# Kernel tuning notes

Hardware: AMD Instinct MI355X
Metric: run time of the kernel (lower is better)

Reference implementation:

```python
import jax, jax.numpy as jnp
import numpy as np

D_IN = 1024
D_OUT = 1024


def setup_inputs() -> dict:
    key = jax.random.key(0)
    kx, kq, kk, kv = jax.random.split(key, 4)
    x = jax.random.normal(kx, (4, 2048, D_IN), dtype=jnp.float32)
    s = 1.0 / np.sqrt(D_IN)
    Wq = jax.random.normal(kq, (D_IN, D_OUT), dtype=jnp.float32) * s
    Wk = jax.random.normal(kk, (D_IN, D_OUT), dtype=jnp.float32) * s
    Wv = jax.random.normal(kv, (D_IN, D_OUT), dtype=jnp.float32) * s
    return {"x": x, "Wq": Wq, "Wk": Wk, "Wv": Wv}


def reference(x, Wq, Wk, Wv):
    # x: [B, S, d_in]; W*: [d_in, d_out]
    B, S, _ = x.shape
    q = x @ Wq  # [B, S, d_out]
    k = x @ Wk
    v = x @ Wv
    scale = 1.0 / jnp.sqrt(jnp.asarray(k.shape[-1], x.dtype))
    scores = jnp.einsum("bqd,bkd->bqk", q, k) * scale  # [B, S, S]
    # causal mask: positions j > i masked to -inf (triu, diagonal=1)
    causal = jnp.tril(jnp.ones((S, S), dtype=bool))
    scores = jnp.where(causal[None, :, :], scores, -jnp.inf)
    attn = jax.nn.softmax(scores, axis=-1)  # dropout p=0.0 -> identity
    return jnp.einsum("bqk,bkd->bqd", attn, v)
```

## Files before the change

### kernel.cpp

```cpp
#include <hip/hip_runtime.h>
#include <hip/hip_bf16.h>

#define NB 4
#define SB 2048
#define DD 1024
#define BM 128
#define BN 128
#define BK 32

typedef __attribute__((ext_vector_type(8))) short bf16x8;
typedef __attribute__((ext_vector_type(4))) short bf16x4;
typedef __attribute__((ext_vector_type(4))) float f32x4;
typedef unsigned int u32;

__device__ __forceinline__ float bf2f(unsigned short u) {
    return __uint_as_float(((u32)u) << 16);
}
__device__ __forceinline__ short f2bf(float f) {
    u32 u = __float_as_uint(f);
    u32 r = (u + 0x7fffu + ((u >> 16) & 1u)) >> 16;
    return (short)r;
}

__device__ __forceinline__ void wait_vm6() {
    asm volatile("s_waitcnt vmcnt(6)" ::: "memory");
}
__device__ __forceinline__ void wait_vm0() {
    asm volatile("s_waitcnt vmcnt(0)" ::: "memory");
}
__device__ __forceinline__ void barrier_raw() {
    __builtin_amdgcn_s_barrier();
    asm volatile("" ::: "memory");
}

__device__ __forceinline__ void mfma_step(const short* As, const short* Bs,
                                          f32x4 (&acc)[4][4], int lane, int wave)
{
    const int wm = (wave >> 1) * 64, wn = (wave & 1) * 64;
    const int fr = lane & 15;
    const int quad = lane >> 4;
    bf16x8 af[4], bf[4];
#pragma unroll
    for (int t = 0; t < 4; t++) {
        af[t] = *(const bf16x8*)&As[(wm + t * 16 + fr) * BK + quad * 8];
        bf[t] = *(const bf16x8*)&Bs[(wn + t * 16 + fr) * BK + quad * 8];
    }
#pragma unroll
    for (int mt = 0; mt < 4; mt++)
#pragma unroll
        for (int nt = 0; nt < 4; nt++)
            acc[mt][nt] = __builtin_amdgcn_mfma_f32_16x16x32_bf16(
                af[mt], bf[nt], acc[mt][nt], 0, 0, 0);
}

__device__ __forceinline__ void mfma_step_pv(const short* As, const short* Bs,
                                             f32x4 (&acc)[2][4], int lane,
                                             int wave)
{
    const int wm = wave * 32;
    const int fr = lane & 15;
    const int quad = lane >> 4;
    bf16x8 af[2], bf[4];
#pragma unroll
    for (int t = 0; t < 2; t++)
        af[t] = *(const bf16x8*)&As[(wm + t * 16 + fr) * BK + quad * 8];
#pragma unroll
    for (int t = 0; t < 4; t++)
        bf[t] = *(const bf16x8*)&Bs[(t * 16 + fr) * BK + quad * 8];
#pragma unroll
    for (int mt = 0; mt < 2; mt++)
#pragma unroll
        for (int nt = 0; nt < 4; nt++)
            acc[mt][nt] = __builtin_amdgcn_mfma_f32_16x16x32_bf16(
                af[mt], bf[nt], acc[mt][nt], 0, 0, 0);
}

__device__ __forceinline__ void stage128x32(const short* __restrict__ g, int ld,
                                            short* lds, int tid) {
    const int wave = tid >> 6, lane = tid & 63;
    const int r = lane >> 2;
    const int c = (lane & 3) * 8;
#pragma unroll
    for (int i = 0; i < 2; i++) {
        const int chunk = wave * 2 + i;
        const short* gp = g + (size_t)(chunk * 16 + r) * ld + c;
        __builtin_amdgcn_global_load_lds(
            (const __attribute__((address_space(1))) u32*)gp,
            (__attribute__((address_space(3))) u32*)(lds + chunk * 512 + lane * 8),
            16, 0, 0);
    }
}

__device__ __forceinline__ void stage64x32(const short* __restrict__ g, int ld,
                                           short* lds, int tid) {
    const int wave = tid >> 6, lane = tid & 63;
    const int r = lane >> 2;
    const int c = (lane & 3) * 8;
    const short* gp = g + (size_t)(wave * 16 + r) * ld + c;
    __builtin_amdgcn_global_load_lds(
        (const __attribute__((address_space(1))) u32*)gp,
        (__attribute__((address_space(3))) u32*)(lds + wave * 512 + lane * 8),
        16, 0, 0);
}

__device__ __forceinline__ void stage_f32_128x32(const float* __restrict__ g,
                                                 int ld, short* lds, int tid) {
    const int r = tid >> 1;
    const int c = (tid & 1) * 16;
    const float* gp = &g[(size_t)r * ld + c];
    float4 v0 = *(const float4*)(gp + 0);
    float4 v1 = *(const float4*)(gp + 4);
    float4 v2 = *(const float4*)(gp + 8);
    float4 v3 = *(const float4*)(gp + 12);
    bf16x8 o0, o1;
    o0[0] = f2bf(v0.x); o0[1] = f2bf(v0.y); o0[2] = f2bf(v0.z); o0[3] = f2bf(v0.w);
    o0[4] = f2bf(v1.x); o0[5] = f2bf(v1.y); o0[6] = f2bf(v1.z); o0[7] = f2bf(v1.w);
    o1[0] = f2bf(v2.x); o1[1] = f2bf(v2.y); o1[2] = f2bf(v2.z); o1[3] = f2bf(v2.w);
    o1[4] = f2bf(v3.x); o1[5] = f2bf(v3.y); o1[6] = f2bf(v3.z); o1[7] = f2bf(v3.w);
    *(bf16x8*)&lds[r * BK + c] = o0;
    *(bf16x8*)&lds[r * BK + c + 8] = o1;
}

__device__ __forceinline__ void gemm_bt_body2(
    const short* __restrict__ A, int lda, const short* __restrict__ Bt, int ldb,
    int m0, int n0, int kend, short* As, short* Bs, f32x4 (&acc)[4][4], int tid)
{
    const int lane = tid & 63;
    const int wave = tid >> 6;
    const short* Ap = A + (size_t)m0 * lda;
    const short* Bp = Bt + (size_t)n0 * ldb;
    for (int k0 = 0; k0 < kend; k0 += 2 * BK) {
        stage128x32(Ap + k0, lda, As, tid);
        stage128x32(Ap + k0 + BK, lda, As + BM * BK, tid);
        stage128x32(Bp + k0, ldb, Bs, tid);
        stage128x32(Bp + k0 + BK, ldb, Bs + BN * BK, tid);
        __syncthreads();
        mfma_step(As, Bs, acc, lane, wave);
        mfma_step(As + BM * BK, Bs + BN * BK, acc, lane, wave);
        __syncthreads();
    }
}

__global__ __launch_bounds__(256) void prep_mm(
    const float* __restrict__ x, const float* __restrict__ Wq,
    const float* __restrict__ Wk, const float* __restrict__ Wv,
    short* __restrict__ xb, short* __restrict__ Wvt, float* __restrict__ Mp4)
{
    __shared__ short As[BM * BK], Bs[BN * BK];
    __shared__ short t[64][65];
    const int bx = blockIdx.x;
    const int tid = threadIdx.x;
    if (bx < 256) {
        const int ch = bx >> 6;
        const int t64 = bx & 63;
        const int m0 = (t64 >> 3) * BM;
        const int n0 = (t64 & 7) * BN;
        const int kbase = ch * 256;
        const int lane = tid & 63, wave = tid >> 6;
        f32x4 acc[4][4];
#pragma unroll
        for (int a = 0; a < 4; a++)
#pragma unroll
            for (int b = 0; b < 4; b++) acc[a][b] = (f32x4){0.f, 0.f, 0.f, 0.f};
        for (int k0 = 0; k0 < 256; k0 += BK) {
            stage_f32_128x32(Wk + (size_t)m0 * DD + kbase + k0, DD, As, tid);
            stage_f32_128x32(Wq + (size_t)n0 * DD + kbase + k0, DD, Bs, tid);
            __syncthreads();
            mfma_step(As, Bs, acc, lane, wave);
            __syncthreads();
        }
        const int wm = (wave >> 1) * 64, wn = (wave & 1) * 64;
        const int fr = lane & 15, quad = lane >> 4;
        float* Mc = Mp4 + (size_t)ch * DD * DD;
#pragma unroll
        for (int mt = 0; mt < 4; mt++)
#pragma unroll
            for (int nt = 0; nt < 4; nt++)
#pragma unroll
                for (int r = 0; r < 4; r++) {
                    const size_t m = m0 + wm + mt * 16 + quad * 4 + r;
                    const size_t n = n0 + wn + nt * 16 + fr;
                    Mc[m * DD + n] = acc[mt][nt][r];
                }
        return;
    }
    if (bx < 4352) {
        const size_t i = ((size_t)(bx - 256) * 256 + tid) * 8;
        float4 a = *(const float4*)&x[i];
        float4 b = *(const float4*)&x[i + 4];
        bf16x8 o;
        o[0] = f2bf(a.x); o[1] = f2bf(a.y); o[2] = f2bf(a.z); o[3] = f2bf(a.w);
        o[4] = f2bf(b.x); o[5] = f2bf(b.y); o[6] = f2bf(b.z); o[7] = f2bf(b.w);
        *(bf16x8*)&xb[i] = o;
        return;
    }
    const int rr = bx - 4352;
    const int k0 = (rr & 15) * 64;
    const int n0 = (rr >> 4) * 64;
    {
        const int r = tid >> 4;
        const int c = (tid & 15) * 4;
#pragma unroll
        for (int i = 0; i < 4; i++) {
            float4 v = *(const float4*)&Wv[(size_t)(k0 + i * 16 + r) * DD + n0 + c];
            t[i * 16 + r][c + 0] = f2bf(v.x);
            t[i * 16 + r][c + 1] = f2bf(v.y);
            t[i * 16 + r][c + 2] = f2bf(v.z);
            t[i * 16 + r][c + 3] = f2bf(v.w);
        }
    }
    __syncthreads();
    {
        const int r = tid >> 3;
        const int c = (tid & 7) * 8;
#pragma unroll
        for (int i = 0; i < 2; i++) {
            bf16x8 o;
#pragma unroll
            for (int j = 0; j < 8; j++) o[j] = t[c + j][i * 32 + r];
            *(bf16x8*)&Wvt[(size_t)(n0 + i * 32 + r) * DD + k0 + c] = o;
        }
    }
}

__global__ __launch_bounds__(256) void mm_reduce(const float* __restrict__ Mp4,
                                                 short* __restrict__ Mp)
{
    const size_t e = ((size_t)blockIdx.x * 256 + threadIdx.x) * 4;
    const size_t N = (size_t)DD * DD;
    float4 s = *(const float4*)&Mp4[e];
#pragma unroll
    for (int c = 1; c < 4; c++) {
        float4 p = *(const float4*)&Mp4[c * N + e];
        s.x += p.x; s.y += p.y; s.z += p.z; s.w += p.w;
    }
    bf16x4 o;
    o[0] = f2bf(s.x); o[1] = f2bf(s.y); o[2] = f2bf(s.z); o[3] = f2bf(s.w);
    *(bf16x4*)&Mp[e] = o;
}

__global__ __launch_bounds__(256) void tv_gemm(
    const short* __restrict__ xb, const short* __restrict__ Mp,
    const short* __restrict__ Wvt, short* __restrict__ T,
    short* __restrict__ Vt)
{
    __shared__ short As[2 * BM * BK], Bs[2 * BN * BK];
    const int lin = blockIdx.x + 8 * blockIdx.y;
    const int swz = (lin & 7) * 64 + (lin >> 3);
    const int n0 = (swz & 7) * BN;
    const int m0 = (swz >> 3) * BM;
    const int isv = blockIdx.z;
    const short* Bt = isv ? Wvt : Mp;
    f32x4 acc[4][4];
#pragma unroll
    for (int a = 0; a < 4; a++)
#pragma unroll
        for (int b = 0; b < 4; b++) acc[a][b] = (f32x4){0.f, 0.f, 0.f, 0.f};
    gemm_bt_body2(xb, DD, Bt, DD, m0, n0, DD, As, Bs, acc, threadIdx.x);
    const int lane = threadIdx.x & 63, wave = threadIdx.x >> 6;
    const int wm = (wave >> 1) * 64, wn = (wave & 1) * 64;
    const int fr = lane & 15, quad = lane >> 4;
    if (!isv) {
#pragma unroll
        for (int mt = 0; mt < 4; mt++)
#pragma unroll
            for (int nt = 0; nt < 4; nt++)
#pragma unroll
                for (int r = 0; r < 4; r++) {
                    const size_t m = m0 + wm + mt * 16 + quad * 4 + r;
                    const size_t n = n0 + wn + nt * 16 + fr;
                    T[m * DD + n] = f2bf(acc[mt][nt][r]);
                }
    } else {
        const int bb = m0 >> 11;
        const int s0 = (m0 & (SB - 1)) + wm + quad * 4;
        short* Vb = Vt + (size_t)bb * DD * SB;
#pragma unroll
        for (int mt = 0; mt < 4; mt++)
#pragma unroll
            for (int nt = 0; nt < 4; nt++) {
                const size_t n = n0 + wn + nt * 16 + fr;
                const size_t s = s0 + mt * 16;
                bf16x4 o;
#pragma unroll
                for (int r = 0; r < 4; r++) o[r] = f2bf(acc[mt][nt][r]);
                *(bf16x4*)&Vb[n * SB + s] = o;
            }
    }
}

__global__ __launch_bounds__(256) void scores_mfma(
    const short* __restrict__ T, const short* __restrict__ xb,
    short* __restrict__ Sc)
{
    const int bx = blockIdx.x;
    const int idx = (bx & 7) * 34 + (bx >> 3);
    int qt = (int)((__fsqrt_rn(4.f * idx + 1.f) - 1.f) * 0.5f);
    while ((qt + 1) * (qt + 2) <= idx) qt++;
    while (qt * (qt + 1) > idx) qt--;
    const int kt = idx - qt * (qt + 1);
    const int qm0 = qt * BM;
    const int kn0 = kt * 64;
    const int b = blockIdx.y;
    __shared__ short As[2 * BM * BK], Bs[2 * 64 * BK];
    const short* Tq = T + (size_t)b * SB * DD + (size_t)qm0 * DD;
    const short* Xk = xb + (size_t)b * SB * DD + (size_t)kn0 * DD;
    short* Sb = Sc + (size_t)b * SB * SB;
    const int tid = threadIdx.x;
    const int lane = tid & 63, wave = tid >> 6;
    f32x4 acc[2][4];
#pragma unroll
    for (int a = 0; a < 2; a++)
#pragma unroll
        for (int c = 0; c < 4; c++) acc[a][c] = (f32x4){0.f, 0.f, 0.f, 0.f};
    for (int k0 = 0; k0 < DD; k0 += 2 * BK) {
        stage128x32(Tq + k0, DD, As, tid);
        stage128x32(Tq + k0 + BK, DD, As + BM * BK, tid);
        stage64x32(Xk + k0, DD, Bs, tid);
        stage64x32(Xk + k0 + BK, DD, Bs + 64 * BK, tid);
        __syncthreads();
        mfma_step_pv(As, Bs, acc, lane, wave);
        mfma_step_pv(As + BM * BK, Bs + 64 * BK, acc, lane, wave);
        __syncthreads();
    }
    const int fr = lane & 15, quad = lane >> 4;
    const float scale = 0.03125f;
#pragma unroll
    for (int mt = 0; mt < 2; mt++)
#pragma unroll
        for (int nt = 0; nt < 4; nt++)
#pragma unroll
            for (int r = 0; r < 4; r++) {
                const size_t q = qm0 + wave * 32 + mt * 16 + quad * 4 + r;
                const size_t k = kn0 + nt * 16 + fr;
                Sb[q * SB + k] = f2bf(acc[mt][nt][r] * scale);
            }
}

__global__ __launch_bounds__(256) void softmax_kernel(short* __restrict__ Sc)
{
    const int row = blockIdx.x;
    const int i = row & (SB - 1);
    const int jlim = ((i >> 7) + 1) << 7;
    short* r = Sc + (size_t)row * SB;
    const int t = threadIdx.x;
    const int lane = t & 63, wave = t >> 6;
    __shared__ float red[8];

    const int j0 = t * 8;
    bf16x8 in = {0, 0, 0, 0, 0, 0, 0, 0};
    if (j0 <= i) in = *(const bf16x8*)&r[j0];
    float v[8];
    float mx = -1e30f;
#pragma unroll
    for (int e = 0; e < 8; e++) {
        const float s = (j0 + e <= i) ? bf2f((unsigned short)in[e]) : -1e30f;
        v[e] = s;
        mx = fmaxf(mx, s);
    }
#pragma unroll
    for (int o = 32; o > 0; o >>= 1) mx = fmaxf(mx, __shfl_down(mx, o));
    if (lane == 0) red[wave] = mx;
    __syncthreads();
    mx = fmaxf(fmaxf(red[0], red[1]), fmaxf(red[2], red[3]));

    float sum = 0.f;
#pragma unroll
    for (int e = 0; e < 8; e++) {
        const float x = (j0 + e <= i) ? __expf(v[e] - mx) : 0.f;
        v[e] = x;
        sum += x;
    }
#pragma unroll
    for (int o = 32; o > 0; o >>= 1) sum += __shfl_down(sum, o);
    if (lane == 0) red[4 + wave] = sum;
    __syncthreads();
    const float inv = 1.0f / (red[4] + red[5] + red[6] + red[7]);
    if (j0 < jlim) {
        bf16x8 o;
#pragma unroll
        for (int e = 0; e < 8; e++) o[e] = f2bf(v[e] * inv);
        *(bf16x8*)&r[j0] = o;
    }
}

__global__ __launch_bounds__(256) void pv_mfma(
    const short* __restrict__ P, const short* __restrict__ Vt,
    float* __restrict__ O)
{
    __shared__ short As[4 * BM * BK];
    __shared__ short Bs[4 * 64 * BK];
    const int n0 = blockIdx.x * 64;
    const int pair = blockIdx.y;
    const int b = blockIdx.z;
    const short* Pb = P + (size_t)b * SB * SB;
    const short* Vb = Vt + (size_t)b * DD * SB;
    float* Ob = O + (size_t)b * SB * DD;
    const int tid = threadIdx.x;
    const int lane = tid & 63, wave = tid >> 6;
    const int fr = lane & 15, quad = lane >> 4;
    for (int half = 0; half < 2; ++half) {
        const int qt = half ? (15 - pair) : pair;
        const int qm0 = qt * BM;
        const int nj = (qt + 1) * 2;
        const short* Pq = Pb + (size_t)qm0 * SB;
        const short* Vn = Vb + (size_t)n0 * SB;
        f32x4 acc[2][4];
#pragma unroll
        for (int a = 0; a < 2; a++)
#pragma unroll
            for (int c = 0; c < 4; c++) acc[a][c] = (f32x4){0.f, 0.f, 0.f, 0.f};
        stage128x32(Pq, SB, As, tid);
        stage128x32(Pq + BK, SB, As + BM * BK, tid);
        stage64x32(Vn, SB, Bs, tid);
        stage64x32(Vn + BK, SB, Bs + 64 * BK, tid);
        for (int j = 0; j < nj; ++j) {
            const int cur = j & 1;
            const short* as = As + cur * (2 * BM * BK);
            const short* bs = Bs + cur * (2 * 64 * BK);
            if (j + 1 < nj) {
                const int off = (j + 1) * 64;
                short* an = As + (cur ^ 1) * (2 * BM * BK);
                short* bn = Bs + (cur ^ 1) * (2 * 64 * BK);
                stage128x32(Pq + off, SB, an, tid);
                stage128x32(Pq + off + BK, SB, an + BM * BK, tid);
                stage64x32(Vn + off, SB, bn, tid);
                stage64x32(Vn + off + BK, SB, bn + 64 * BK, tid);
                wait_vm6();
            } else {
                wait_vm0();
            }
            barrier_raw();
            mfma_step_pv(as, bs, acc, lane, wave);
            mfma_step_pv(as + BM * BK, bs + 64 * BK, acc, lane, wave);
            barrier_raw();
        }
#pragma unroll
        for (int mt = 0; mt < 2; mt++)
#pragma unroll
            for (int nt = 0; nt < 4; nt++)
#pragma unroll
                for (int r = 0; r < 4; r++) {
                    const size_t q = qm0 + wave * 32 + mt * 16 + quad * 4 + r;
                    const size_t n = n0 + nt * 16 + fr;
                    Ob[q * DD + n] = acc[mt][nt][r];
                }
    }
}

extern "C" void kernel_launch(void* const* d_in, const int* in_sizes, int n_in,
                              void* d_out, int out_size, void* d_ws, size_t ws_size,
                              hipStream_t stream)
{
    const float* x  = (const float*)d_in[0];
    const float* Wq = (const float*)d_in[1];
    const float* Wk = (const float*)d_in[2];
    const float* Wv = (const float*)d_in[3];
    float* out = (float*)d_out;

    const size_t XE = (size_t)NB * SB * DD;
    const size_t WE = (size_t)DD * DD;
    short* xb  = (short*)d_ws;
    short* T   = xb + XE;
    short* Vt  = T + XE;
    short* Sc  = Vt + XE;
    float* Pp  = (float*)(Sc + (size_t)NB * SB * SB);
    short* Wvt = (short*)(Pp + (size_t)NB * 1024 * DD);
    short* Mp  = Wvt + WE;
    float* Mp4 = (float*)Sc;

    prep_mm<<<dim3(256 + 4096 + 256), 256, 0, stream>>>(
        x, Wq, Wk, Wv, xb, Wvt, Mp4);
    mm_reduce<<<dim3(1024), 256, 0, stream>>>(Mp4, Mp);
    tv_gemm<<<dim3(DD / BN, (NB * SB) / BM, 2), 256, 0, stream>>>(
        xb, Mp, Wvt, T, Vt);
    scores_mfma<<<dim3(272, NB), 256, 0, stream>>>(T, xb, Sc);
    softmax_kernel<<<dim3(NB * SB), 256, 0, stream>>>(Sc);
    pv_mfma<<<dim3(DD / 64, 8, NB), 256, 0, stream>>>(Sc, Vt, out);
}
```

Baseline: 231.0 us.

## Retile the projection GEMM to 256x128 with a three-stage async LDS pipeline

The projection GEMM kernel moves from 128x128 tiles with 256 threads to 256x128 tiles with 512 threads (8 waves). Each stage now holds a 64-wide K slice, and the stages rotate through three LDS buffers. Global-to-LDS loads for step j+2 are issued before computing step j, using counted vmcnt waits instead of a full sync. The MFMA section runs at raised wave priority. The aim is to hide global load latency and improve operand reuse, at the cost of about 147KB of LDS, which allows only one block per CU.

```diff
diff --git a/kernel.cpp b/kernel.cpp
--- a/kernel.cpp
+++ b/kernel.cpp
@@ -22,6 +22,9 @@
     return (short)r;
 }
 
+__device__ __forceinline__ void wait_vm12() {
+    asm volatile("s_waitcnt vmcnt(12)" ::: "memory");
+}
 __device__ __forceinline__ void wait_vm6() {
     asm volatile("s_waitcnt vmcnt(6)" ::: "memory");
 }
@@ -101,6 +104,35 @@
         (const __attribute__((address_space(1))) u32*)gp,
         (__attribute__((address_space(3))) u32*)(lds + wave * 512 + lane * 8),
         16, 0, 0);
+}
+
+__device__ __forceinline__ void stage_tile256(const short* __restrict__ gA,
+                                              int lda,
+                                              const short* __restrict__ gB,
+                                              int ldb, short* slot, int tid) {
+    const int w = tid >> 6, l = tid & 63;
+    const int lr = l >> 2;
+    const int lc = (l & 3) * 8;
+#pragma unroll
+    for (int i = 0; i < 4; i++) {
+        const int ks = i >> 1;
+        const int row = (i & 1) * 128 + w * 16 + lr;
+        const short* gp = gA + (size_t)row * lda + ks * 32 + lc;
+        __builtin_amdgcn_global_load_lds(
+            (const __attribute__((address_space(1))) u32*)gp,
+            (__attribute__((address_space(3))) u32*)(slot + i * 4096 + w * 512 + l * 8),
+            16, 0, 0);
+    }
+    short* bbase = slot + 16384;
+#pragma unroll
+    for (int i = 0; i < 2; i++) {
+        const int row = w * 16 + lr;
+        const short* gp = gB + (size_t)row * ldb + i * 32 + lc;
+        __builtin_amdgcn_global_load_lds(
+            (const __attribute__((address_space(1))) u32*)gp,
+            (__attribute__((address_space(3))) u32*)(bbase + i * 4096 + w * 512 + l * 8),
+            16, 0, 0);
+    }
 }
 
 __device__ __forceinline__ void stage_f32_128x32(const float* __restrict__ g,
@@ -121,26 +153,6 @@
     *(bf16x8*)&lds[r * BK + c + 8] = o1;
 }
 
-__device__ __forceinline__ void gemm_bt_body2(
-    const short* __restrict__ A, int lda, const short* __restrict__ Bt, int ldb,
-    int m0, int n0, int kend, short* As, short* Bs, f32x4 (&acc)[4][4], int tid)
-{
-    const int lane = tid & 63;
-    const int wave = tid >> 6;
-    const short* Ap = A + (size_t)m0 * lda;
-    const short* Bp = Bt + (size_t)n0 * ldb;
-    for (int k0 = 0; k0 < kend; k0 += 2 * BK) {
-        stage128x32(Ap + k0, lda, As, tid);
-        stage128x32(Ap + k0 + BK, lda, As + BM * BK, tid);
-        stage128x32(Bp + k0, ldb, Bs, tid);
-        stage128x32(Bp + k0 + BK, ldb, Bs + BN * BK, tid);
-        __syncthreads();
-        mfma_step(As, Bs, acc, lane, wave);
-        mfma_step(As + BM * BK, Bs + BN * BK, acc, lane, wave);
-        __syncthreads();
-    }
-}
-
 __global__ __launch_bounds__(256) void prep_mm(
     const float* __restrict__ x, const float* __restrict__ Wq,
     const float* __restrict__ Wk, const float* __restrict__ Wv,
@@ -239,25 +251,46 @@
     *(bf16x4*)&Mp[e] = o;
 }
 
-__global__ __launch_bounds__(256) void tv_gemm(
+__global__ __launch_bounds__(512) void tv_gemm(
     const short* __restrict__ xb, const short* __restrict__ Mp,
     const short* __restrict__ Wvt, short* __restrict__ T,
     short* __restrict__ Vt)
 {
-    __shared__ short As[2 * BM * BK], Bs[2 * BN * BK];
+    __shared__ short lds[3 * 24576];
     const int lin = blockIdx.x + 8 * blockIdx.y;
-    const int swz = (lin & 7) * 64 + (lin >> 3);
-    const int n0 = (swz & 7) * BN;
-    const int m0 = (swz >> 3) * BM;
+    const int swz = (lin & 7) * 32 + (lin >> 3);
+    const int n0 = (swz & 7) * 128;
+    const int m0 = (swz >> 3) * 256;
     const int isv = blockIdx.z;
     const short* Bt = isv ? Wvt : Mp;
+    const short* Ap = xb + (size_t)m0 * DD;
+    const short* Bp = Bt + (size_t)n0 * DD;
+    const int tid = threadIdx.x;
+    const int lane = tid & 63, wave = tid >> 6;
     f32x4 acc[4][4];
 #pragma unroll
     for (int a = 0; a < 4; a++)
 #pragma unroll
         for (int b = 0; b < 4; b++) acc[a][b] = (f32x4){0.f, 0.f, 0.f, 0.f};
-    gemm_bt_body2(xb, DD, Bt, DD, m0, n0, DD, As, Bs, acc, threadIdx.x);
-    const int lane = threadIdx.x & 63, wave = threadIdx.x >> 6;
+
+    stage_tile256(Ap, DD, Bp, DD, lds, tid);
+    stage_tile256(Ap + 64, DD, Bp + 64, DD, lds + 24576, tid);
+    for (int j = 0; j < 16; ++j) {
+        if (j < 14)
+            stage_tile256(Ap + (j + 2) * 64, DD, Bp + (j + 2) * 64, DD,
+                          lds + ((j + 2) % 3) * 24576, tid);
+        if (j < 14)       wait_vm12();
+        else if (j == 14) wait_vm6();
+        else              wait_vm0();
+        barrier_raw();
+        short* slot = lds + (j % 3) * 24576;
+        __builtin_amdgcn_s_setprio(1);
+        mfma_step(slot, slot + 16384, acc, lane, wave);
+        mfma_step(slot + 8192, slot + 16384 + 4096, acc, lane, wave);
+        __builtin_amdgcn_s_setprio(0);
+        barrier_raw();
+    }
+
     const int wm = (wave >> 1) * 64, wn = (wave & 1) * 64;
     const int fr = lane & 15, quad = lane >> 4;
     if (!isv) {
@@ -472,8 +505,7 @@
     prep_mm<<<dim3(256 + 4096 + 256), 256, 0, stream>>>(
         x, Wq, Wk, Wv, xb, Wvt, Mp4);
     mm_reduce<<<dim3(1024), 256, 0, stream>>>(Mp4, Mp);
-    tv_gemm<<<dim3(DD / BN, (NB * SB) / BM, 2), 256, 0, stream>>>(
-        xb, Mp, Wvt, T, Vt);
+    tv_gemm<<<dim3(8, 32, 2), 512, 0, stream>>>(xb, Mp, Wvt, T, Vt);
     scores_mfma<<<dim3(272, NB), 256, 0, stream>>>(T, xb, Sc);
     softmax_kernel<<<dim3(NB * SB), 256, 0, stream>>>(Sc);
     pv_mfma<<<dim3(DD / 64, 8, NB), 256, 0, stream>>>(Sc, Vt, out);
```

New measurement: 231.2 us. Within noise of the previous version (+0.1%).
